# Performance work log

Measured on AMD Instinct MI355X. Metric: run time of the kernel, lower is better.

The kernel has to match this reference:

```python
import jax, jax.numpy as jnp
import numpy as np

N_NODES = 50000
N_EDGES = 800000
D = 128          # node_state_dim
H = 256          # edge hidden / message dim (= 2*D)
NH = 256         # node MLP hidden


def setup_inputs() -> dict:
    key = jax.random.key(0)
    ks = jax.random.split(key, 20)
    s = 0.05
    inp = {
        "node_states": jax.random.normal(ks[0], (N_NODES, D), jnp.float32),
        "edge_features": jax.random.normal(ks[1], (N_EDGES, 1), jnp.float32),
        "from_idx": jax.random.randint(ks[2], (N_EDGES,), 0, N_NODES, jnp.int32),
        "to_idx": jax.random.randint(ks[3], (N_EDGES,), 0, N_NODES, jnp.int32),
        # forward-direction message net: Linear(2D+1 -> H), ReLU, Linear(H -> H)
        "W1": jax.random.normal(ks[4], (2 * D + 1, H), jnp.float32) * s,
        "b1": jnp.zeros((H,), jnp.float32),
        "W2": jax.random.normal(ks[5], (H, H), jnp.float32) * s,
        "b2": jnp.zeros((H,), jnp.float32),
        # reverse-direction message net (separate params)
        "RW1": jax.random.normal(ks[6], (2 * D + 1, H), jnp.float32) * s,
        "Rb1": jnp.zeros((H,), jnp.float32),
        "RW2": jax.random.normal(ks[7], (H, H), jnp.float32) * s,
        "Rb2": jnp.zeros((H,), jnp.float32),
        # node update MLP: Linear(3D -> NH), ReLU, Linear(NH -> D)
        "Wn1": jax.random.normal(ks[8], (3 * D, NH), jnp.float32) * s,
        "bn1": jnp.zeros((NH,), jnp.float32),
        "Wn2": jax.random.normal(ks[9], (NH, D), jnp.float32) * s,
        "bn2": jnp.zeros((D,), jnp.float32),
    }
    return inp


def _mlp2(x, W1, b1, W2, b2):
    return jax.nn.relu(x @ W1 + b1) @ W2 + b2


def reference(node_states, edge_features, from_idx, to_idx,
              W1, b1, W2, b2, RW1, Rb1, RW2, Rb2, Wn1, bn1, Wn2, bn2):
    n_nodes = node_states.shape[0]
    from_states = node_states[from_idx]            # [E, D]
    to_states = node_states[to_idx]                # [E, D]

    # forward direction: messages go to to_idx
    edge_in = jnp.concatenate([from_states, to_states, edge_features], axis=-1)  # [E, 2D+1]
    msgs = _mlp2(edge_in, W1, b1, W2, b2)                                        # [E, H]
    agg = jax.ops.segment_sum(msgs, to_idx, num_segments=n_nodes)                # [N, H]

    # reverse direction: swap roles, aggregate onto from_idx
    redge_in = jnp.concatenate([to_states, from_states, edge_features], axis=-1)
    rmsgs = _mlp2(redge_in, RW1, Rb1, RW2, Rb2)
    agg = agg + jax.ops.segment_sum(rmsgs, from_idx, num_segments=n_nodes)

    # residual node update: MLP on [agg, node_states] -> [N, D]
    upd_in = jnp.concatenate([agg, node_states], axis=-1)                        # [N, 3D]
    return node_states + _mlp2(upd_in, Wn1, bn1, Wn2, bn2)
```

## Files before the change

### kernel.cpp

```cpp
#include <hip/hip_runtime.h>
#include <hip/hip_bf16.h>


typedef __bf16 bf16;
typedef __attribute__((ext_vector_type(8))) __bf16 bf16x8;
typedef __attribute__((ext_vector_type(4))) __bf16 bf16x4v;
typedef __attribute__((ext_vector_type(4))) float floatx4;
typedef __attribute__((ext_vector_type(2))) float floatx2;

#define DD 128
#define HH 256
#define CAPB 800
#define MAXBINS 3200

__device__ __forceinline__ bf16x8 ns8(const float* __restrict__ NS, int row, int col, int N) {
    bf16x8 v;
    if (row < N) {
        float4 f0 = *(const float4*)&NS[(size_t)row * DD + col];
        float4 f1 = *(const float4*)&NS[(size_t)row * DD + col + 4];
        v[0] = (bf16)f0.x; v[1] = (bf16)f0.y; v[2] = (bf16)f0.z; v[3] = (bf16)f0.w;
        v[4] = (bf16)f1.x; v[5] = (bf16)f1.y; v[6] = (bf16)f1.z; v[7] = (bf16)f1.w;
    } else {
        v = (bf16x8)(bf16)0.0f;
    }
    return v;
}

__global__ void k_pre(const float* __restrict__ W1, const float* __restrict__ RW1,
                      bf16* __restrict__ Wt1, int* __restrict__ gcur, int NBINS) {
    const int b = blockIdx.x, t = threadIdx.x;
    if (b < 512) {
        int idx = b * 256 + t;
        int n = idx >> 7, k = idx & 127;
        float v;
        if (n < 256)      v = W1[k * 256 + n];
        else if (n < 512) v = W1[(128 + k) * 256 + (n - 256)];
        else if (n < 768) v = RW1[k * 256 + (n - 512)];
        else              v = RW1[(128 + k) * 256 + (n - 768)];
        Wt1[idx] = (bf16)v;
    } else {
        int i = (b - 512) * 256 + t;
        if (i < NBINS) gcur[i] = 0;
    }
}

__global__ __launch_bounds__(256) void k_front(
    const float* __restrict__ NS, const int* __restrict__ from_idx,
    const int* __restrict__ to_idx, const float* __restrict__ ef,
    const float* __restrict__ W2, const float* __restrict__ RW2,
    const float* __restrict__ Wn1, const float* __restrict__ Wn2,
    const float* __restrict__ b2, const float* __restrict__ Rb2,
    const bf16* __restrict__ Wt1,
    int* __restrict__ gcur, int2* __restrict__ binbuf,
    unsigned char* __restrict__ Pn, bf16* __restrict__ Pf,
    bf16* __restrict__ Wth, bf16* __restrict__ Wt2,
    float* __restrict__ u, float* __restrict__ ru,
    int E, int N, int NP, int NBINS, int BINB, int MB) {
    __shared__ __align__(16) unsigned char smem[25600];
    const int b = blockIdx.x, t = threadIdx.x;

    if (b < BINB) {
        int* hist = (int*)smem;
        int* base = hist + MAXBINS;
        const int NBF = NP >> 5;
        for (int i = t; i < NBINS; i += 256) hist[i] = 0;
        __syncthreads();
        const int e0 = b * 2048;
        int f[8], tt[8]; float w[8]; bool valid[8];
#pragma unroll
        for (int q = 0; q < 8; ++q) {
            int e = e0 + q * 256 + t;
            valid[q] = e < E;
            int ec = valid[q] ? e : 0;
            f[q] = from_idx[ec]; tt[q] = to_idx[ec]; w[q] = ef[ec];
        }
#pragma unroll
        for (int q = 0; q < 8; ++q) {
            if (valid[q]) {
                atomicAdd(&hist[tt[q] >> 5], 1);
                atomicAdd(&hist[NBF + (f[q] >> 5)], 1);
            }
        }
        __syncthreads();
        for (int i = t; i < NBINS; i += 256) {
            int h = hist[i];
            base[i] = h ? atomicAdd(&gcur[i], h) : 0;
            hist[i] = 0;
        }
        __syncthreads();
#pragma unroll
        for (int q = 0; q < 8; ++q) {
            if (valid[q]) {
                int wb = __float_as_int(w[q]);
                int b1 = tt[q] >> 5;
                int r1 = base[b1] + atomicAdd(&hist[b1], 1);
                if (r1 < CAPB)
                    binbuf[(size_t)b1 * CAPB + r1] = make_int2(((tt[q] & 31) << 17) | f[q], wb);
                int b2i = NBF + (f[q] >> 5);
                int r2 = base[b2i] + atomicAdd(&hist[b2i], 1);
                if (r2 < CAPB)
                    binbuf[(size_t)b2i * CAPB + r2] = make_int2(((f[q] & 31) << 17) | tt[q], wb);
            }
        }
        return;
    }

    if (b < BINB + 769) {
        int bb = b - BINB;
        if (bb < 640) {
            int k = bb, m = t;
            float v;
            if (k < 512) {
                const float* Wsrc = (k < 256) ? W2 : RW2;
                int i = k & 255;
                float acc = 0.f;
                for (int j = 0; j < 256; ++j) acc += Wsrc[i * 256 + j] * Wn1[j * 256 + m];
                v = acc;
            } else {
                v = Wn1[(256 + k - 512) * 256 + m];
            }
            Wth[m * 640 + k] = (bf16)v;
        } else if (bb < 768) {
            int idx = (bb - 640) * 256 + t;
            int n = idx >> 8, k = idx & 255;
            Wt2[idx] = (bf16)Wn2[k * 128 + n];
        } else {
            int m = t;
            float a = 0.f, c2 = 0.f;
            for (int j = 0; j < 256; ++j) {
                float w = Wn1[j * 256 + m];
                a += b2[j] * w;
                c2 += Rb2[j] * w;
            }
            u[m] = a;
            ru[m] = c2;
        }
        return;
    }

    {
        bf16 (*As)[64][40] = (bf16(*)[64][40])smem;
        bf16 (*Bs)[64][40] = (bf16(*)[64][40])(smem + 10240);
        const int p = b - (BINB + 769);
        const int row0 = (p >> 4) * 64;
        const int col0 = (p & 15) * 64;
        const int wv = t >> 6, lane = t & 63;
        const int l15 = lane & 15, quad = lane >> 4;
        const int srow = t >> 2, kc = (t & 3) * 8;
        floatx4 acc[4] = {};
        for (int k0 = 0; k0 < DD; k0 += 64) {
            bf16x8 av0 = ns8(NS, row0 + srow, k0 + kc, N);
            bf16x8 av1 = ns8(NS, row0 + srow, k0 + 32 + kc, N);
            bf16x8 bv0 = *(const bf16x8*)&Wt1[(size_t)(col0 + srow) * DD + k0 + kc];
            bf16x8 bv1 = *(const bf16x8*)&Wt1[(size_t)(col0 + srow) * DD + k0 + 32 + kc];
            __syncthreads();
            *(bf16x8*)&As[0][srow][kc] = av0;
            *(bf16x8*)&As[1][srow][kc] = av1;
            *(bf16x8*)&Bs[0][srow][kc] = bv0;
            *(bf16x8*)&Bs[1][srow][kc] = bv1;
            __syncthreads();
#pragma unroll
            for (int h = 0; h < 2; ++h) {
                bf16x8 bfr = *(const bf16x8*)&Bs[h][wv * 16 + l15][quad * 8];
#pragma unroll
                for (int r = 0; r < 4; ++r) {
                    bf16x8 afr = *(const bf16x8*)&As[h][r * 16 + l15][quad * 8];
                    acc[r] = __builtin_amdgcn_mfma_f32_16x16x32_bf16(afr, bfr, acc[r], 0, 0, 0);
                }
            }
        }
        const int ocol = col0 + wv * 16 + l15;
        const int ch = ocol & 255;
        const int half = (ocol >> 9) & 1;
        const bool isNbr = ((ocol >> 8) & 1) == 0;
#pragma unroll
        for (int r = 0; r < 4; ++r)
#pragma unroll
            for (int i = 0; i < 4; ++i) {
                int orow = row0 + r * 16 + quad * 4 + i;
                float v = acc[r][i];
                if (isNbr) {
                    int pk = __builtin_amdgcn_cvt_pk_fp8_f32(v, v, 0, false);
                    Pn[(size_t)orow * 512 + half * 256 + ch] = (unsigned char)(pk & 0xFF);
                } else {
                    Pf[(size_t)orow * 512 + half * 256 + ch] = (bf16)v;
                }
            }
    }
}

__global__ __launch_bounds__(256) void k_aggf(
    const unsigned char* __restrict__ Pn, const bf16* __restrict__ Pf,
    const int2* __restrict__ binbuf, const int* __restrict__ gcnt,
    const float* __restrict__ W1, const float* __restrict__ b1,
    const float* __restrict__ RW1, const float* __restrict__ Rb1,
    bf16* __restrict__ S_to, bf16* __restrict__ S_fr,
    int* __restrict__ deg, int NP) {
    __shared__ int hist[32], kstart[32], cur[32], scanbuf[32];
    __shared__ int2 srec[CAPB];
    const int b = blockIdx.x, t = threadIdx.x;
    const int NBF = NP >> 5;
    const bool rev = b >= NBF;
    const int node0 = (rev ? b - NBF : b) << 5;
    int cnt = gcnt[b]; if (cnt > CAPB) cnt = CAPB;
    const int2* bin = binbuf + (size_t)b * CAPB;
    if (t < 32) hist[t] = 0;
    __syncthreads();
    for (int i = t; i < cnt; i += 256)
        atomicAdd(&hist[((unsigned)bin[i].x) >> 17], 1);
    __syncthreads();
    if (t < 32) scanbuf[t] = hist[t];
    __syncthreads();
    for (int d = 1; d < 32; d <<= 1) {
        int v = (t < 32 && t >= d) ? scanbuf[t - d] : 0;
        __syncthreads();
        if (t < 32) scanbuf[t] += v;
        __syncthreads();
    }
    if (t < 32) { kstart[t] = scanbuf[t] - hist[t]; cur[t] = scanbuf[t] - hist[t]; }
    __syncthreads();
    for (int i = t; i < cnt; i += 256) {
        int2 r = bin[i];
        int rk = atomicAdd(&cur[((unsigned)r.x) >> 17], 1);
        srec[rk] = r;
    }
    __syncthreads();
    const int wv = t >> 6, lane = t & 63, c = lane * 4;
    const int fixoff = rev ? 256 : 0;
    const int nbroff = rev ? 256 : 0;
    const float* bb = rev ? Rb1 : b1;
    const float* wl = (rev ? RW1 : W1) + 65536;
    float4 bv = *(const float4*)&bb[c];
    float4 wv4 = *(const float4*)&wl[c];
    bf16* Sarr = rev ? S_fr : S_to;
    for (int key = wv; key < 32; key += 4) {
        int node = node0 + key;
        bf16x4v pf = *(const bf16x4v*)&Pf[(size_t)node * 512 + fixoff + c];
        float fx0 = (float)pf[0] + bv.x;
        float fx1 = (float)pf[1] + bv.y;
        float fx2 = (float)pf[2] + bv.z;
        float fx3 = (float)pf[3] + bv.w;
        int beg = kstart[key], kc2 = hist[key], end = beg + kc2;
        float a0 = 0.f, a1 = 0.f, a2 = 0.f, a3 = 0.f;
        int j = beg;
        for (; j + 8 <= end; j += 8) {
            int2 rr[8]; int qq[8];
#pragma unroll
            for (int z = 0; z < 8; ++z) rr[z] = srec[j + z];
#pragma unroll
            for (int z = 0; z < 8; ++z)
                qq[z] = *(const int*)&Pn[(size_t)(rr[z].x & 0x1FFFF) * 512 + nbroff + c];
#pragma unroll
            for (int z = 0; z < 8; ++z) {
                float w = __int_as_float(rr[z].y);
                floatx2 lo = __builtin_amdgcn_cvt_pk_f32_fp8(qq[z], false);
                floatx2 hi = __builtin_amdgcn_cvt_pk_f32_fp8(qq[z], true);
                a0 += fmaxf(fx0 + lo.x + w * wv4.x, 0.f);
                a1 += fmaxf(fx1 + lo.y + w * wv4.y, 0.f);
                a2 += fmaxf(fx2 + hi.x + w * wv4.z, 0.f);
                a3 += fmaxf(fx3 + hi.y + w * wv4.w, 0.f);
            }
        }
        for (; j < end; ++j) {
            int2 r = srec[j];
            int qq = *(const int*)&Pn[(size_t)(r.x & 0x1FFFF) * 512 + nbroff + c];
            float w = __int_as_float(r.y);
            floatx2 lo = __builtin_amdgcn_cvt_pk_f32_fp8(qq, false);
            floatx2 hi = __builtin_amdgcn_cvt_pk_f32_fp8(qq, true);
            a0 += fmaxf(fx0 + lo.x + w * wv4.x, 0.f);
            a1 += fmaxf(fx1 + lo.y + w * wv4.y, 0.f);
            a2 += fmaxf(fx2 + hi.x + w * wv4.z, 0.f);
            a3 += fmaxf(fx3 + hi.y + w * wv4.w, 0.f);
        }
        bf16x4v o;
        o[0] = (bf16)a0; o[1] = (bf16)a1; o[2] = (bf16)a2; o[3] = (bf16)a3;
        *(bf16x4v*)&Sarr[(size_t)node * 256 + c] = o;
        if (lane == 0) deg[(rev ? NP : 0) + node] = kc2;
    }
}

__global__ __launch_bounds__(256) void k_node(
    const bf16* __restrict__ S_to, const bf16* __restrict__ S_fr,
    const float* __restrict__ NS, const bf16* __restrict__ Wth,
    const bf16* __restrict__ Wt2,
    const float* __restrict__ u, const float* __restrict__ ru,
    const float* __restrict__ bn1, const float* __restrict__ bn2,
    const int* __restrict__ deg, float* __restrict__ out, int NP, int N) {
    __shared__ __align__(16) unsigned char smem[51200];
    bf16 (*As)[64][40]  = (bf16(*)[64][40])smem;
    bf16 (*Bs)[256][40] = (bf16(*)[256][40])(smem + 10240);
    bf16 (*Hs)[264] = (bf16(*)[264])smem;
    const int tid = threadIdx.x;
    const int wv = tid >> 6, lane = tid & 63;
    const int l15 = lane & 15, quad = lane >> 4;
    const int row0 = blockIdx.x * 64;
    const int srow4 = tid >> 2, kc = (tid & 3) * 8;
    floatx4 acc[4][4] = {};
    const int arow = row0 + srow4;
    auto loadA = [&](int k) -> bf16x8 {
        if (k < 512) {
            const bf16* S = (k < 256) ? S_to : S_fr;
            return *(const bf16x8*)&S[(size_t)arow * 256 + (k & 255) + kc];
        }
        return ns8(NS, arow, (k - 512) + kc, N);
    };
    for (int k0 = 0; k0 < 640; k0 += 64) {
        bf16x8 av0 = loadA(k0);
        bf16x8 av1 = loadA(k0 + 32);
        bf16x8 bv[2][4];
#pragma unroll
        for (int h = 0; h < 2; ++h)
#pragma unroll
            for (int j = 0; j < 4; ++j)
                bv[h][j] = *(const bf16x8*)&Wth[(size_t)(srow4 + 64 * j) * 640 + k0 + h * 32 + kc];
        __syncthreads();
        *(bf16x8*)&As[0][srow4][kc] = av0;
        *(bf16x8*)&As[1][srow4][kc] = av1;
#pragma unroll
        for (int h = 0; h < 2; ++h)
#pragma unroll
            for (int j = 0; j < 4; ++j)
                *(bf16x8*)&Bs[h][srow4 + 64 * j][kc] = bv[h][j];
        __syncthreads();
#pragma unroll
        for (int h = 0; h < 2; ++h)
#pragma unroll
            for (int s = 0; s < 4; ++s) {
                bf16x8 bfr = *(const bf16x8*)&Bs[h][wv * 64 + s * 16 + l15][quad * 8];
#pragma unroll
                for (int r = 0; r < 4; ++r) {
                    bf16x8 afr = *(const bf16x8*)&As[h][r * 16 + l15][quad * 8];
                    acc[s][r] = __builtin_amdgcn_mfma_f32_16x16x32_bf16(afr, bfr, acc[s][r], 0, 0, 0);
                }
            }
    }
    __syncthreads();
#pragma unroll
    for (int s = 0; s < 4; ++s) {
        int col = wv * 64 + s * 16 + l15;
        float uc = u[col], rc = ru[col], bc = bn1[col];
#pragma unroll
        for (int r = 0; r < 4; ++r)
#pragma unroll
            for (int i = 0; i < 4; ++i) {
                int row = r * 16 + quad * 4 + i;
                float v = acc[s][r][i] + (float)deg[row0 + row] * uc
                        + (float)deg[NP + row0 + row] * rc + bc;
                Hs[row][col] = (bf16)fmaxf(v, 0.f);
            }
    }
    __syncthreads();
    floatx4 acc2[2][4] = {};
    for (int k0 = 0; k0 < HH; k0 += 32) {
        bf16x8 afr[4];
#pragma unroll
        for (int r = 0; r < 4; ++r)
            afr[r] = *(const bf16x8*)&Hs[r * 16 + l15][k0 + quad * 8];
#pragma unroll
        for (int s = 0; s < 2; ++s) {
            int col = wv * 32 + s * 16 + l15;
            bf16x8 bfr = *(const bf16x8*)&Wt2[(size_t)col * HH + k0 + quad * 8];
#pragma unroll
            for (int r = 0; r < 4; ++r)
                acc2[s][r] = __builtin_amdgcn_mfma_f32_16x16x32_bf16(afr[r], bfr, acc2[s][r], 0, 0, 0);
        }
    }
#pragma unroll
    for (int s = 0; s < 2; ++s) {
        int ocol = wv * 32 + s * 16 + l15;
        float bb = bn2[ocol];
#pragma unroll
        for (int r = 0; r < 4; ++r)
#pragma unroll
            for (int i = 0; i < 4; ++i) {
                int orow = row0 + r * 16 + quad * 4 + i;
                if (orow < N)
                    out[(size_t)orow * DD + ocol] = acc2[s][r][i] + bb + NS[(size_t)orow * DD + ocol];
            }
    }
}

extern "C" void kernel_launch(void* const* d_in, const int* in_sizes, int n_in,
                              void* d_out, int out_size, void* d_ws, size_t ws_size,
                              hipStream_t stream) {
    const float* NS   = (const float*)d_in[0];
    const float* ef   = (const float*)d_in[1];
    const int* from_idx = (const int*)d_in[2];
    const int* to_idx   = (const int*)d_in[3];
    const float* W1  = (const float*)d_in[4];
    const float* b1  = (const float*)d_in[5];
    const float* W2  = (const float*)d_in[6];
    const float* b2  = (const float*)d_in[7];
    const float* RW1 = (const float*)d_in[8];
    const float* Rb1 = (const float*)d_in[9];
    const float* RW2 = (const float*)d_in[10];
    const float* Rb2 = (const float*)d_in[11];
    const float* Wn1 = (const float*)d_in[12];
    const float* bn1 = (const float*)d_in[13];
    const float* Wn2 = (const float*)d_in[14];
    const float* bn2 = (const float*)d_in[15];

    const int N  = in_sizes[0] / DD;
    const int E  = in_sizes[2];
    const int NP = ((N + 63) / 64) * 64;
    const int MB = NP / 64;
    const int NBF = NP / 32;
    const int NBINS = 2 * NBF;
    const int BINB = (E + 2047) / 2048;
    const int FRONT = BINB + 769 + 16 * MB;
    const int PREB = 512 + (NBINS + 255) / 256;

    char* base = (char*)d_ws;
    size_t off_b = 0;
    auto alloc = [&](size_t b) { size_t o = off_b; off_b += (b + 255) & ~(size_t)255; return o; };
    unsigned char* Pn = (unsigned char*)(base + alloc((size_t)NP * 512));
    bf16* Pf   = (bf16*)(base + alloc((size_t)NP * 512 * 2));
    bf16* S_to = (bf16*)(base + alloc((size_t)NP * 256 * 2));
    bf16* S_fr = (bf16*)(base + alloc((size_t)NP * 256 * 2));
    int* deg   = (int*)(base + alloc((size_t)2 * NP * 4));
    int* gcur  = (int*)(base + alloc((size_t)NBINS * 4));
    int2* binbuf = (int2*)(base + alloc((size_t)NBINS * CAPB * 8));
    bf16* Wt1 = (bf16*)(base + alloc(1024 * 128 * 2));
    bf16* Wth = (bf16*)(base + alloc(256 * 640 * 2));
    bf16* Wt2 = (bf16*)(base + alloc(128 * 256 * 2));
    float* u  = (float*)(base + alloc(256 * 4));
    float* ru = (float*)(base + alloc(256 * 4));

    k_pre<<<PREB, 256, 0, stream>>>(W1, RW1, Wt1, gcur, NBINS);
    k_front<<<FRONT, 256, 0, stream>>>(NS, from_idx, to_idx, ef,
                                       W2, RW2, Wn1, Wn2, b2, Rb2, Wt1,
                                       gcur, binbuf, Pn, Pf, Wth, Wt2, u, ru,
                                       E, N, NP, NBINS, BINB, MB);
    k_aggf<<<NBINS, 256, 0, stream>>>(Pn, Pf, binbuf, gcur, W1, b1, RW1, Rb1,
                                      S_to, S_fr, deg, NP);
    k_node<<<MB, 256, 0, stream>>>(S_to, S_fr, NS, Wth, Wt2, u, ru, bn1, bn2,
                                   deg, (float*)d_out, NP, N);
}
```

Baseline: 329.4 us.

## Widen front projection tiles to 128 columns and halve node GEMM K-step

In the front kernel, each projection block now computes a 64x128 output tile instead of 64x64. A-fragments loaded from shared memory are reused across two B sub-tiles, which halves the number of projection blocks and the redundant reads of node states. In the node kernel, the first GEMM now steps K by 32 instead of 64, shrinking shared memory from 51200 to 33792 bytes so more blocks can be resident per CU. The cost is twice as many barrier-separated iterations in the node GEMM, plus more accumulator registers and larger shared memory in the front kernel.

Measured after the change: 320.7 us. 1.03x faster.

```diff
diff --git a/kernel.cpp b/kernel.cpp
--- a/kernel.cpp
+++ b/kernel.cpp
@@ -56,7 +56,7 @@
     bf16* __restrict__ Wth, bf16* __restrict__ Wt2,
     float* __restrict__ u, float* __restrict__ ru,
     int E, int N, int NP, int NBINS, int BINB, int MB) {
-    __shared__ __align__(16) unsigned char smem[25600];
+    __shared__ __align__(16) unsigned char smem[30720];
     const int b = blockIdx.x, t = threadIdx.x;
 
     if (b < BINB) {
@@ -140,52 +140,64 @@
 
     {
         bf16 (*As)[64][40] = (bf16(*)[64][40])smem;
-        bf16 (*Bs)[64][40] = (bf16(*)[64][40])(smem + 10240);
+        bf16 (*Bs)[2][64][40] = (bf16(*)[2][64][40])(smem + 10240);
         const int p = b - (BINB + 769);
-        const int row0 = (p >> 4) * 64;
-        const int col0 = (p & 15) * 64;
+        const int row0 = (p >> 3) * 64;
+        const int colp = (p & 7) * 128;
         const int wv = t >> 6, lane = t & 63;
         const int l15 = lane & 15, quad = lane >> 4;
         const int srow = t >> 2, kc = (t & 3) * 8;
-        floatx4 acc[4] = {};
+        floatx4 acc[2][4] = {};
         for (int k0 = 0; k0 < DD; k0 += 64) {
             bf16x8 av0 = ns8(NS, row0 + srow, k0 + kc, N);
             bf16x8 av1 = ns8(NS, row0 + srow, k0 + 32 + kc, N);
-            bf16x8 bv0 = *(const bf16x8*)&Wt1[(size_t)(col0 + srow) * DD + k0 + kc];
-            bf16x8 bv1 = *(const bf16x8*)&Wt1[(size_t)(col0 + srow) * DD + k0 + 32 + kc];
+            bf16x8 bv00 = *(const bf16x8*)&Wt1[(size_t)(colp + srow) * DD + k0 + kc];
+            bf16x8 bv01 = *(const bf16x8*)&Wt1[(size_t)(colp + srow) * DD + k0 + 32 + kc];
+            bf16x8 bv10 = *(const bf16x8*)&Wt1[(size_t)(colp + 64 + srow) * DD + k0 + kc];
+            bf16x8 bv11 = *(const bf16x8*)&Wt1[(size_t)(colp + 64 + srow) * DD + k0 + 32 + kc];
             __syncthreads();
             *(bf16x8*)&As[0][srow][kc] = av0;
             *(bf16x8*)&As[1][srow][kc] = av1;
-            *(bf16x8*)&Bs[0][srow][kc] = bv0;
-            *(bf16x8*)&Bs[1][srow][kc] = bv1;
+            *(bf16x8*)&Bs[0][0][srow][kc] = bv00;
+            *(bf16x8*)&Bs[0][1][srow][kc] = bv01;
+            *(bf16x8*)&Bs[1][0][srow][kc] = bv10;
+            *(bf16x8*)&Bs[1][1][srow][kc] = bv11;
             __syncthreads();
 #pragma unroll
             for (int h = 0; h < 2; ++h) {
-                bf16x8 bfr = *(const bf16x8*)&Bs[h][wv * 16 + l15][quad * 8];
-#pragma unroll
-                for (int r = 0; r < 4; ++r) {
-                    bf16x8 afr = *(const bf16x8*)&As[h][r * 16 + l15][quad * 8];
-                    acc[r] = __builtin_amdgcn_mfma_f32_16x16x32_bf16(afr, bfr, acc[r], 0, 0, 0);
+                bf16x8 afr[4];
+#pragma unroll
+                for (int r = 0; r < 4; ++r)
+                    afr[r] = *(const bf16x8*)&As[h][r * 16 + l15][quad * 8];
+#pragma unroll
+                for (int cp = 0; cp < 2; ++cp) {
+                    bf16x8 bfr = *(const bf16x8*)&Bs[cp][h][wv * 16 + l15][quad * 8];
+#pragma unroll
+                    for (int r = 0; r < 4; ++r)
+                        acc[cp][r] = __builtin_amdgcn_mfma_f32_16x16x32_bf16(afr[r], bfr, acc[cp][r], 0, 0, 0);
                 }
             }
         }
-        const int ocol = col0 + wv * 16 + l15;
-        const int ch = ocol & 255;
-        const int half = (ocol >> 9) & 1;
-        const bool isNbr = ((ocol >> 8) & 1) == 0;
-#pragma unroll
-        for (int r = 0; r < 4; ++r)
-#pragma unroll
-            for (int i = 0; i < 4; ++i) {
-                int orow = row0 + r * 16 + quad * 4 + i;
-                float v = acc[r][i];
-                if (isNbr) {
-                    int pk = __builtin_amdgcn_cvt_pk_fp8_f32(v, v, 0, false);
-                    Pn[(size_t)orow * 512 + half * 256 + ch] = (unsigned char)(pk & 0xFF);
-                } else {
-                    Pf[(size_t)orow * 512 + half * 256 + ch] = (bf16)v;
+#pragma unroll
+        for (int cp = 0; cp < 2; ++cp) {
+            const int ocol = colp + cp * 64 + wv * 16 + l15;
+            const int ch = ocol & 255;
+            const int half = (ocol >> 9) & 1;
+            const bool isNbr = ((ocol >> 8) & 1) == 0;
+#pragma unroll
+            for (int r = 0; r < 4; ++r)
+#pragma unroll
+                for (int i = 0; i < 4; ++i) {
+                    int orow = row0 + r * 16 + quad * 4 + i;
+                    float v = acc[cp][r][i];
+                    if (isNbr) {
+                        int pk = __builtin_amdgcn_cvt_pk_fp8_f32(v, v, 0, false);
+                        Pn[(size_t)orow * 512 + half * 256 + ch] = (unsigned char)(pk & 0xFF);
+                    } else {
+                        Pf[(size_t)orow * 512 + half * 256 + ch] = (bf16)v;
+                    }
                 }
-            }
+        }
     }
 }
 
@@ -286,53 +298,44 @@
     const float* __restrict__ u, const float* __restrict__ ru,
     const float* __restrict__ bn1, const float* __restrict__ bn2,
     const int* __restrict__ deg, float* __restrict__ out, int NP, int N) {
-    __shared__ __align__(16) unsigned char smem[51200];
-    bf16 (*As)[64][40]  = (bf16(*)[64][40])smem;
-    bf16 (*Bs)[256][40] = (bf16(*)[256][40])(smem + 10240);
+    __shared__ __align__(16) unsigned char smem[33792];
+    bf16 (*As)[40]  = (bf16(*)[40])smem;
+    bf16 (*Bs)[40]  = (bf16(*)[40])(smem + 5120);
     bf16 (*Hs)[264] = (bf16(*)[264])smem;
     const int tid = threadIdx.x;
     const int wv = tid >> 6, lane = tid & 63;
     const int l15 = lane & 15, quad = lane >> 4;
     const int row0 = blockIdx.x * 64;
-    const int srow4 = tid >> 2, kc = (tid & 3) * 8;
+    const int srow = tid >> 2, kc = (tid & 3) * 8;
     floatx4 acc[4][4] = {};
-    const int arow = row0 + srow4;
-    auto loadA = [&](int k) -> bf16x8 {
-        if (k < 512) {
-            const bf16* S = (k < 256) ? S_to : S_fr;
-            return *(const bf16x8*)&S[(size_t)arow * 256 + (k & 255) + kc];
-        }
-        return ns8(NS, arow, (k - 512) + kc, N);
-    };
-    for (int k0 = 0; k0 < 640; k0 += 64) {
-        bf16x8 av0 = loadA(k0);
-        bf16x8 av1 = loadA(k0 + 32);
-        bf16x8 bv[2][4];
-#pragma unroll
-        for (int h = 0; h < 2; ++h)
-#pragma unroll
-            for (int j = 0; j < 4; ++j)
-                bv[h][j] = *(const bf16x8*)&Wth[(size_t)(srow4 + 64 * j) * 640 + k0 + h * 32 + kc];
-        __syncthreads();
-        *(bf16x8*)&As[0][srow4][kc] = av0;
-        *(bf16x8*)&As[1][srow4][kc] = av1;
-#pragma unroll
-        for (int h = 0; h < 2; ++h)
-#pragma unroll
-            for (int j = 0; j < 4; ++j)
-                *(bf16x8*)&Bs[h][srow4 + 64 * j][kc] = bv[h][j];
-        __syncthreads();
-#pragma unroll
-        for (int h = 0; h < 2; ++h)
-#pragma unroll
-            for (int s = 0; s < 4; ++s) {
-                bf16x8 bfr = *(const bf16x8*)&Bs[h][wv * 64 + s * 16 + l15][quad * 8];
-#pragma unroll
-                for (int r = 0; r < 4; ++r) {
-                    bf16x8 afr = *(const bf16x8*)&As[h][r * 16 + l15][quad * 8];
-                    acc[s][r] = __builtin_amdgcn_mfma_f32_16x16x32_bf16(afr, bfr, acc[s][r], 0, 0, 0);
-                }
-            }
+    const int arow = row0 + srow;
+    for (int k0 = 0; k0 < 640; k0 += 32) {
+        bf16x8 av;
+        if (k0 < 512) {
+            const bf16* S = (k0 < 256) ? S_to : S_fr;
+            av = *(const bf16x8*)&S[(size_t)arow * 256 + (k0 & 255) + kc];
+        } else {
+            av = ns8(NS, arow, (k0 - 512) + kc, N);
+        }
+        bf16x8 bv[4];
+#pragma unroll
+        for (int j = 0; j < 4; ++j)
+            bv[j] = *(const bf16x8*)&Wth[(size_t)(srow + 64 * j) * 640 + k0 + kc];
+        __syncthreads();
+        *(bf16x8*)&As[srow][kc] = av;
+#pragma unroll
+        for (int j = 0; j < 4; ++j)
+            *(bf16x8*)&Bs[srow + 64 * j][kc] = bv[j];
+        __syncthreads();
+#pragma unroll
+        for (int s = 0; s < 4; ++s) {
+            bf16x8 bfr = *(const bf16x8*)&Bs[wv * 64 + s * 16 + l15][quad * 8];
+#pragma unroll
+            for (int r = 0; r < 4; ++r) {
+                bf16x8 afr = *(const bf16x8*)&As[r * 16 + l15][quad * 8];
+                acc[s][r] = __builtin_amdgcn_mfma_f32_16x16x32_bf16(afr, bfr, acc[s][r], 0, 0, 0);
+            }
+        }
     }
     __syncthreads();
 #pragma unroll
@@ -407,7 +410,7 @@
     const int NBF = NP / 32;
     const int NBINS = 2 * NBF;
     const int BINB = (E + 2047) / 2048;
-    const int FRONT = BINB + 769 + 16 * MB;
+    const int FRONT = BINB + 769 + 8 * MB;
     const int PREB = 512 + (NBINS + 255) / 256;
 
     char* base = (char*)d_ws;
```
